# Kernel tuning notes

Measured on AMD Instinct MI355X. Metric: run time of the kernel, lower is better.

The kernel has to match this reference:

```python
import jax, jax.numpy as jnp
import numpy as np

N, F, H = 22, 448, 64
LN_EPS = 1e-5


def _layernorm(h, g, b):
    mu = h.mean(axis=-1, keepdims=True)
    var = ((h - mu) ** 2).mean(axis=-1, keepdims=True)
    return (h - mu) / jnp.sqrt(var + LN_EPS) * g + b


def setup_inputs() -> dict:
    key = jax.random.key(0)
    ks = jax.random.split(key, 16)
    B = 128
    x = jax.random.normal(ks[0], (B, N, F), dtype=jnp.float32)
    s = lambda fan_in: 1.0 / np.sqrt(fan_in)
    # correlation-branch edge_weight_net: Linear(2F,64) -> ReLU -> Linear(64,1) -> Sigmoid
    cw1 = jax.random.uniform(ks[1], (2 * F, 64), jnp.float32, -s(2 * F), s(2 * F))
    cb1 = jax.random.uniform(ks[2], (64,), jnp.float32, -s(2 * F), s(2 * F))
    cw2 = jax.random.uniform(ks[3], (64, 1), jnp.float32, -s(64), s(64))
    cb2 = jax.random.uniform(ks[4], (1,), jnp.float32, -s(64), s(64))
    # semantic branch
    emb = jax.random.normal(ks[5], (N, H), dtype=jnp.float32) * 0.01
    D = 2 * H + 2 * F
    sw1 = jax.random.uniform(ks[6], (D, H), jnp.float32, -s(D), s(D))
    sb1 = jax.random.uniform(ks[7], (H,), jnp.float32, -s(D), s(D))
    ln_g = jnp.ones((H,), jnp.float32)
    ln_b = jnp.zeros((H,), jnp.float32)
    sw2 = jax.random.uniform(ks[8], (H, H // 2), jnp.float32, -s(H), s(H))
    sb2 = jax.random.uniform(ks[9], (H // 2,), jnp.float32, -s(H), s(H))
    sw3 = jax.random.uniform(ks[10], (H // 2, 1), jnp.float32, -s(H // 2), s(H // 2))
    sb3 = jax.random.uniform(ks[11], (1,), jnp.float32, -s(H // 2), s(H // 2))
    thr = jnp.asarray(0.3, jnp.float32)
    alpha_p = jnp.asarray(0.6, jnp.float32)
    return dict(x=x, cw1=cw1, cb1=cb1, cw2=cw2, cb2=cb2, emb=emb,
                sw1=sw1, sb1=sb1, ln_g=ln_g, ln_b=ln_b,
                sw2=sw2, sb2=sb2, sw3=sw3, sb3=sb3,
                thr=thr, alpha_p=alpha_p)


def reference(x, cw1, cb1, cw2, cb2, emb, sw1, sb1, ln_g, ln_b,
              sw2, sb2, sw3, sb3, thr, alpha_p):
    B, n, f = x.shape
    eye = jnp.eye(n, dtype=x.dtype)[None]

    # ---- Correlation graph ----
    xc = x - x.mean(axis=-1, keepdims=True)
    std = jnp.std(x, axis=-1, ddof=1, keepdims=True) + 1e-8  # torch std is unbiased
    xn = xc / std
    corr = jnp.abs(jnp.einsum('bif,bjf->bij', xn, xn) / f)
    # pairwise edge features (B,N,N,2F)
    xi = jnp.broadcast_to(x[:, :, None, :], (B, n, n, f))
    xj = jnp.broadcast_to(x[:, None, :, :], (B, n, n, f))
    ef = jnp.concatenate([xi, xj], axis=-1)
    h = jax.nn.relu(ef @ cw1 + cb1)
    w_corr = jax.nn.sigmoid((h @ cw2 + cb2)[..., 0])
    g_corr = corr * w_corr + eye

    # ---- Semantic graph ----
    ei = jnp.broadcast_to(emb[None, :, None, :], (B, n, n, H))
    ej = jnp.broadcast_to(emb[None, None, :, :], (B, n, n, H))
    sf = jnp.concatenate([ei, ej, xi, xj], axis=-1)  # (B,N,N,2H+2F)
    h1 = jax.nn.relu(_layernorm(sf @ sw1 + sb1, ln_g, ln_b))
    h2 = jax.nn.relu(h1 @ sw2 + sb2)
    w_sem = jax.nn.sigmoid((h2 @ sw3 + sb3)[..., 0])  # (B,N,N)
    # original loop fills only i<j and mirrors; diagonal stays 0
    upper = jnp.triu(w_sem, k=1)
    adj = upper + jnp.swapaxes(upper, 1, 2)
    t = jax.nn.sigmoid(thr)
    adj = jnp.where(adj > t, adj, jnp.zeros_like(adj))
    g_sem = adj + eye

    # ---- Learned fusion ----
    alpha = jax.nn.sigmoid(alpha_p)
    return alpha * g_corr + (1.0 - alpha) * g_sem
```

## Files before the change

kernel.cpp:

```cpp
#include <hip/hip_runtime.h>
#include <math.h>

namespace {
constexpr int kN = 22;
constexpr int kF = 448;
constexpr int kNP = kN * kN;
constexpr int kXStr = 452;
constexpr int kSm1 = kN * kXStr + 2 * kN;
constexpr int kAStr = 36;
constexpr int kBStr = 68;
constexpr int kPStr = 68;
}

__global__ __launch_bounds__(256) void hgc_k1(
    const float* __restrict__ x,
    const float* __restrict__ cw1, const float* __restrict__ cb1,
    const float* __restrict__ emb,
    const float* __restrict__ sw1, const float* __restrict__ sb1,
    float* __restrict__ C, float* __restrict__ g,
    int M, int Mtiles, int nGemm)
{
    __shared__ __align__(16) float sm[kSm1];
    const int tid = threadIdx.x;

    if ((int)blockIdx.x < nGemm) {
        float* As = sm;
        float* Bs = sm + 64 * kAStr;
        const int bm = blockIdx.x % Mtiles;
        const int bn = blockIdx.x / Mtiles;
        const int m0 = bm * 32;

        const float* Wsrc =
            (bn == 0) ? cw1 :
            (bn == 1) ? cw1 + 448 * 64 :
            (bn == 2) ? sw1 + 128 * 64 :
                        sw1 + 576 * 64;

        const int tm = tid & 15;
        const int tn = tid >> 4;
        float acc[2][4];
        #pragma unroll
        for (int i = 0; i < 2; ++i)
            #pragma unroll
            for (int j = 0; j < 4; ++j) acc[i][j] = 0.f;

        for (int k0 = 0; k0 < kF; k0 += 64) {
            #pragma unroll
            for (int pass = 0; pass < 2; ++pass) {
                const int idx = tid + pass * 256;
                const int row = idx >> 4, kq = idx & 15;
                const int m = m0 + row;
                float4 v = {0, 0, 0, 0};
                if (m < M) v = *(const float4*)&x[(size_t)m * kF + k0 + kq * 4];
                As[(kq * 4 + 0) * kAStr + row] = v.x;
                As[(kq * 4 + 1) * kAStr + row] = v.y;
                As[(kq * 4 + 2) * kAStr + row] = v.z;
                As[(kq * 4 + 3) * kAStr + row] = v.w;
            }
            #pragma unroll
            for (int pass = 0; pass < 4; ++pass) {
                const int idx = tid + pass * 256;
                const int k = idx >> 4, nq = idx & 15;
                const float4 v = *(const float4*)&Wsrc[(size_t)(k0 + k) * 64 + nq * 4];
                *(float4*)&Bs[k * kBStr + nq * 4] = v;
            }
            __syncthreads();
            #pragma unroll 8
            for (int k = 0; k < 64; ++k) {
                const float2 a2 = *(const float2*)&As[k * kAStr + tm * 2];
                const float4 b4 = *(const float4*)&Bs[k * kBStr + tn * 4];
                acc[0][0] = fmaf(a2.x, b4.x, acc[0][0]);
                acc[0][1] = fmaf(a2.x, b4.y, acc[0][1]);
                acc[0][2] = fmaf(a2.x, b4.z, acc[0][2]);
                acc[0][3] = fmaf(a2.x, b4.w, acc[0][3]);
                acc[1][0] = fmaf(a2.y, b4.x, acc[1][0]);
                acc[1][1] = fmaf(a2.y, b4.y, acc[1][1]);
                acc[1][2] = fmaf(a2.y, b4.z, acc[1][2]);
                acc[1][3] = fmaf(a2.y, b4.w, acc[1][3]);
            }
            __syncthreads();
        }

        if (bn >= 2) {
            const float* W2 = sw1 + (bn == 2 ? 0 : 64) * 64;
            #pragma unroll
            for (int pass = 0; pass < 2; ++pass) {
                const int idx = tid + pass * 256;
                const int row = idx >> 4, kq = idx & 15;
                const int r = (m0 + row) % kN;
                const float4 v = *(const float4*)&emb[(size_t)r * 64 + kq * 4];
                As[(kq * 4 + 0) * kAStr + row] = v.x;
                As[(kq * 4 + 1) * kAStr + row] = v.y;
                As[(kq * 4 + 2) * kAStr + row] = v.z;
                As[(kq * 4 + 3) * kAStr + row] = v.w;
            }
            #pragma unroll
            for (int pass = 0; pass < 4; ++pass) {
                const int idx = tid + pass * 256;
                const int k = idx >> 4, nq = idx & 15;
                const float4 v = *(const float4*)&W2[(size_t)k * 64 + nq * 4];
                *(float4*)&Bs[k * kBStr + nq * 4] = v;
            }
            __syncthreads();
            #pragma unroll 8
            for (int k = 0; k < 64; ++k) {
                const float2 a2 = *(const float2*)&As[k * kAStr + tm * 2];
                const float4 b4 = *(const float4*)&Bs[k * kBStr + tn * 4];
                acc[0][0] = fmaf(a2.x, b4.x, acc[0][0]);
                acc[0][1] = fmaf(a2.x, b4.y, acc[0][1]);
                acc[0][2] = fmaf(a2.x, b4.z, acc[0][2]);
                acc[0][3] = fmaf(a2.x, b4.w, acc[0][3]);
                acc[1][0] = fmaf(a2.y, b4.x, acc[1][0]);
                acc[1][1] = fmaf(a2.y, b4.y, acc[1][1]);
                acc[1][2] = fmaf(a2.y, b4.z, acc[1][2]);
                acc[1][3] = fmaf(a2.y, b4.w, acc[1][3]);
            }
        }

        float4 bias = {0, 0, 0, 0};
        if (bn == 0)      bias = *(const float4*)&cb1[tn * 4];
        else if (bn == 2) bias = *(const float4*)&sb1[tn * 4];
        #pragma unroll
        for (int i = 0; i < 2; ++i) {
            const int m = m0 + tm * 2 + i;
            if (m < M) {
                float4 o;
                o.x = acc[i][0] + bias.x; o.y = acc[i][1] + bias.y;
                o.z = acc[i][2] + bias.z; o.w = acc[i][3] + bias.w;
                *(float4*)&C[(size_t)m * 256 + bn * 64 + tn * 4] = o;
            }
        }
    } else {
        float* smu = sm + kN * kXStr;
        float* sis = smu + kN;
        const int cb = blockIdx.x - nGemm;
        const int b = cb >> 1;
        const int r0 = (cb & 1) * 11;

        const float4* xb4 = (const float4*)(x + (size_t)b * (kN * kF));
        for (int idx = tid; idx < kN * kF / 4; idx += 256) {
            const float4 v = xb4[idx];
            const int r = idx / 112;
            const int k = (idx - r * 112) * 4;
            float* d = sm + r * kXStr + k;
            d[0] = v.x; d[1] = v.y; d[2] = v.z; d[3] = v.w;
        }
        __syncthreads();

        {
            const int wid = tid >> 6, lane = tid & 63;
            for (int r = wid; r < kN; r += 4) {
                const float* row = sm + r * kXStr;
                float s = 0.f;
                #pragma unroll
                for (int c = 0; c < 7; ++c) s += row[c * 64 + lane];
                #pragma unroll
                for (int o = 32; o; o >>= 1) s += __shfl_xor(s, o, 64);
                const float mean = s * (1.f / 448.f);
                float ss = 0.f;
                #pragma unroll
                for (int c = 0; c < 7; ++c) { const float d = row[c * 64 + lane] - mean; ss = fmaf(d, d, ss); }
                #pragma unroll
                for (int o = 32; o; o >>= 1) ss += __shfl_xor(ss, o, 64);
                if (lane == 0) {
                    smu[r] = mean;
                    sis[r] = 1.f / (sqrtf(ss * (1.f / 447.f)) + 1e-8f);
                }
            }
        }
        __syncthreads();

        for (int p = tid; p < 11 * kN; p += 256) {
            const int pi = p / 22;
            const int i = r0 + pi, j = p - pi * 22;
            const float4* ri = (const float4*)(sm + i * kXStr);
            const float4* rj = (const float4*)(sm + j * kXStr);
            float dot = 0.f;
            for (int q = 0; q < 112; ++q) {
                const float4 a = ri[q], bq = rj[q];
                dot = fmaf(a.x, bq.x, dot); dot = fmaf(a.y, bq.y, dot);
                dot = fmaf(a.z, bq.z, dot); dot = fmaf(a.w, bq.w, dot);
            }
            const float c = (dot - 448.f * smu[i] * smu[j]) * sis[i] * sis[j] * (1.f / 448.f);
            g[(size_t)b * kNP + i * 22 + j] = fabsf(c);
        }
    }
}

__global__ __launch_bounds__(256) void hgc_k2(
    const float* __restrict__ C, const float* __restrict__ g,
    const float* __restrict__ cw2, const float* __restrict__ cb2,
    const float* __restrict__ sw2, const float* __restrict__ sb2,
    const float* __restrict__ sw3, const float* __restrict__ sb3,
    const float* __restrict__ ln_g, const float* __restrict__ ln_b,
    const float* __restrict__ thr, const float* __restrict__ alpha_p,
    float* __restrict__ out)
{
    __shared__ __align__(16) float sp[4 * kN * kPStr];
    __shared__ float sg[kNP];
    __shared__ __align__(16) float sw2s[2048];
    __shared__ float scw2[64], slng[64], slnb[64], ssw3[32], ssb2[32];
    __shared__ float vbuf[32 * 66];

    const int tid = threadIdx.x;
    const int b   = blockIdx.x >> 2;
    const int pb  = blockIdx.x & 3;

    #pragma unroll
    for (int a = 0; a < 4; ++a) {
        float* dst = sp + a * kN * kPStr;
        for (int idx = tid; idx < 352; idx += 256) {
            const int r = idx >> 4, kq = idx & 15;
            const float4 v = *(const float4*)&C[((size_t)(b * 22 + r)) * 256 + a * 64 + kq * 4];
            *(float4*)&dst[r * kPStr + kq * 4] = v;
        }
    }
    for (int idx = tid; idx < kNP; idx += 256) sg[idx] = g[(size_t)b * kNP + idx];
    {
        const float4* s4 = (const float4*)sw2;
        for (int idx = tid; idx < 512; idx += 256)
            *((float4*)(sw2s + idx * 4)) = s4[idx];
    }
    if (tid < 64)       { scw2[tid] = cw2[tid]; slng[tid] = ln_g[tid]; slnb[tid] = ln_b[tid]; }
    else if (tid < 96)  { ssw3[tid - 64] = sw3[tid - 64]; }
    else if (tid < 128) { ssb2[tid - 96] = sb2[tid - 96]; }
    __syncthreads();

    const int pl = tid >> 3;
    const int t  = tid & 7;
    const float* sa1 = sp;
    const float* sa2 = sp + kN * kPStr;
    const float* su1 = sp + 2 * kN * kPStr;
    const float* su2 = sp + 3 * kN * kPStr;

    for (int ch = 0; ch < 4; ++ch) {
        const int lp = ch * 32 + pl;
        const bool valid = lp < 121;
        const int p = valid ? (pb * 121 + lp) : 0;
        const int i = p / 22, j = p - (p / 22) * 22;

        float zc = 0.f;
        {
            const float* pa1 = sa1 + i * kPStr + t * 8;
            const float* pa2 = sa2 + j * kPStr + t * 8;
            #pragma unroll
            for (int c = 0; c < 8; ++c) {
                const float h = fmaxf(pa1[c] + pa2[c], 0.f);
                zc = fmaf(h, scw2[t * 8 + c], zc);
            }
            zc += __shfl_xor(zc, 1, 64); zc += __shfl_xor(zc, 2, 64); zc += __shfl_xor(zc, 4, 64);
        }
        const float wc = 1.f / (1.f + __expf(-(zc + cb2[0])));

        const int lo = (i < j) ? i : j, hi = (i < j) ? j : i;
        const float* pu1 = su1 + lo * kPStr + t * 8;
        const float* pu2 = su2 + hi * kPStr + t * 8;
        float raw[8];
        float s1 = 0.f;
        #pragma unroll
        for (int c = 0; c < 8; ++c) { raw[c] = pu1[c] + pu2[c]; s1 += raw[c]; }
        s1 += __shfl_xor(s1, 1, 64); s1 += __shfl_xor(s1, 2, 64); s1 += __shfl_xor(s1, 4, 64);
        const float mean = s1 * (1.f / 64.f);
        float s2 = 0.f;
        #pragma unroll
        for (int c = 0; c < 8; ++c) { const float d = raw[c] - mean; s2 = fmaf(d, d, s2); }
        s2 += __shfl_xor(s2, 1, 64); s2 += __shfl_xor(s2, 2, 64); s2 += __shfl_xor(s2, 4, 64);
        const float rstd = rsqrtf(s2 * (1.f / 64.f) + 1e-5f);
        {
            float* vb = vbuf + pl * 66 + t * 8;
            #pragma unroll
            for (int c = 0; c < 8; ++c) {
                const int k = t * 8 + c;
                float v = (raw[c] - mean) * rstd;
                v = fmaf(v, slng[k], slnb[k]);
                vb[c] = fmaxf(v, 0.f);
            }
        }
        __syncthreads();

        float4 acc = {0, 0, 0, 0};
        {
            const float* vb = vbuf + pl * 66;
            for (int k = 0; k < 64; ++k) {
                const float v = vb[k];
                const float4 w = *((const float4*)(sw2s + k * 32 + t * 4));
                acc.x = fmaf(v, w.x, acc.x); acc.y = fmaf(v, w.y, acc.y);
                acc.z = fmaf(v, w.z, acc.z); acc.w = fmaf(v, w.w, acc.w);
            }
        }
        float z2;
        {
            const int o0 = t * 4;
            z2  = fmaxf(acc.x + ssb2[o0 + 0], 0.f) * ssw3[o0 + 0];
            z2 += fmaxf(acc.y + ssb2[o0 + 1], 0.f) * ssw3[o0 + 1];
            z2 += fmaxf(acc.z + ssb2[o0 + 2], 0.f) * ssw3[o0 + 2];
            z2 += fmaxf(acc.w + ssb2[o0 + 3], 0.f) * ssw3[o0 + 3];
            z2 += __shfl_xor(z2, 1, 64); z2 += __shfl_xor(z2, 2, 64); z2 += __shfl_xor(z2, 4, 64);
        }

        if (valid && t == 0) {
            float gsem;
            if (i == j) {
                gsem = 1.f;
            } else {
                const float wsem = 1.f / (1.f + expf(-(z2 + sb3[0])));
                const float tt   = 1.f / (1.f + expf(-thr[0]));
                gsem = (wsem > tt) ? wsem : 0.f;
            }
            const float alpha = 1.f / (1.f + __expf(-alpha_p[0]));
            const float gcorr = fmaf(sg[p], wc, (i == j) ? 1.f : 0.f);
            out[(size_t)b * kNP + p] = fmaf(alpha, gcorr, (1.f - alpha) * gsem);
        }
    }
}

extern "C" void kernel_launch(void* const* d_in, const int* in_sizes, int n_in,
                              void* d_out, int out_size, void* d_ws, size_t ws_size,
                              hipStream_t stream)
{
    (void)n_in; (void)out_size; (void)ws_size;
    const float* x     = (const float*)d_in[0];
    const float* cw1   = (const float*)d_in[1];
    const float* cb1   = (const float*)d_in[2];
    const float* cw2   = (const float*)d_in[3];
    const float* cb2   = (const float*)d_in[4];
    const float* emb   = (const float*)d_in[5];
    const float* sw1   = (const float*)d_in[6];
    const float* sb1   = (const float*)d_in[7];
    const float* ln_g  = (const float*)d_in[8];
    const float* ln_b  = (const float*)d_in[9];
    const float* sw2   = (const float*)d_in[10];
    const float* sb2   = (const float*)d_in[11];
    const float* sw3   = (const float*)d_in[12];
    const float* sb3   = (const float*)d_in[13];
    const float* thr   = (const float*)d_in[14];
    const float* alpha = (const float*)d_in[15];
    float* out = (float*)d_out;
    float* ws  = (float*)d_ws;

    const int B = in_sizes[0] / (kN * kF);
    const int M = kN * B;
    const int Mtiles = (M + 31) / 32;
    const int nGemm = Mtiles * 4;

    float* C = ws;
    float* g = ws + (size_t)M * 256;

    hipLaunchKernelGGL(hgc_k1, dim3(nGemm + 2 * B), dim3(256), 0, stream,
                       x, cw1, cb1, emb, sw1, sb1, C, g, M, Mtiles, nGemm);
    hipLaunchKernelGGL(hgc_k2, dim3(4 * B), dim3(256), 0, stream,
                       C, g, cw2, cb2, sw2, sb2, sw3, sb3, ln_g, ln_b, thr, alpha, out);
}
```

Before: 125.5 us.

## Enlarge GEMM tile with register prefetch and exploit pair symmetry in both kernels

After: 135.1 us. 1.08x slower.

```diff
diff --git a/kernel.cpp b/kernel.cpp
--- a/kernel.cpp
+++ b/kernel.cpp
@@ -7,9 +7,10 @@
 constexpr int kNP = kN * kN;
 constexpr int kXStr = 452;
 constexpr int kSm1 = kN * kXStr + 2 * kN;
-constexpr int kAStr = 36;
+constexpr int kAStr = 68;
 constexpr int kBStr = 68;
 constexpr int kPStr = 68;
+constexpr int kVStr = 68;
 }
 
 __global__ __launch_bounds__(256) void hgc_k1(
@@ -28,7 +29,7 @@
         float* Bs = sm + 64 * kAStr;
         const int bm = blockIdx.x % Mtiles;
         const int bn = blockIdx.x / Mtiles;
-        const int m0 = bm * 32;
+        const int m0 = bm * 64;
 
         const float* Wsrc =
             (bn == 0) ? cw1 :
@@ -38,82 +39,93 @@
 
         const int tm = tid & 15;
         const int tn = tid >> 4;
-        float acc[2][4];
+        const int ld_row = tid >> 4;
+        const int ld_kq  = tid & 15;
+
+        float acc[4][4];
         #pragma unroll
-        for (int i = 0; i < 2; ++i)
+        for (int i = 0; i < 4; ++i)
             #pragma unroll
             for (int j = 0; j < 4; ++j) acc[i][j] = 0.f;
 
+        float4 rA[4], rB[4];
+        #pragma unroll
+        for (int p = 0; p < 4; ++p) {
+            const int row = ld_row + p * 16;
+            int m = m0 + row; if (m >= M) m = M - 1;
+            rA[p] = *(const float4*)&x[(size_t)m * kF + ld_kq * 4];
+            rB[p] = *(const float4*)&Wsrc[(size_t)row * 64 + ld_kq * 4];
+        }
+
         for (int k0 = 0; k0 < kF; k0 += 64) {
             #pragma unroll
-            for (int pass = 0; pass < 2; ++pass) {
-                const int idx = tid + pass * 256;
-                const int row = idx >> 4, kq = idx & 15;
-                const int m = m0 + row;
-                float4 v = {0, 0, 0, 0};
-                if (m < M) v = *(const float4*)&x[(size_t)m * kF + k0 + kq * 4];
-                As[(kq * 4 + 0) * kAStr + row] = v.x;
-                As[(kq * 4 + 1) * kAStr + row] = v.y;
-                As[(kq * 4 + 2) * kAStr + row] = v.z;
-                As[(kq * 4 + 3) * kAStr + row] = v.w;
-            }
+            for (int p = 0; p < 4; ++p) {
+                const int row = ld_row + p * 16;
+                As[(ld_kq * 4 + 0) * kAStr + row] = rA[p].x;
+                As[(ld_kq * 4 + 1) * kAStr + row] = rA[p].y;
+                As[(ld_kq * 4 + 2) * kAStr + row] = rA[p].z;
+                As[(ld_kq * 4 + 3) * kAStr + row] = rA[p].w;
+                *(float4*)&Bs[row * kBStr + ld_kq * 4] = rB[p];
+            }
+            __syncthreads();
+            const int kn = k0 + 64;
+            if (kn < kF) {
+                #pragma unroll
+                for (int p = 0; p < 4; ++p) {
+                    const int row = ld_row + p * 16;
+                    int m = m0 + row; if (m >= M) m = M - 1;
+                    rA[p] = *(const float4*)&x[(size_t)m * kF + kn + ld_kq * 4];
+                    rB[p] = *(const float4*)&Wsrc[(size_t)(kn + row) * 64 + ld_kq * 4];
+                }
+            } else if (bn >= 2) {
+                const float* W2 = sw1 + (bn == 2 ? 0 : 64) * 64;
+                #pragma unroll
+                for (int p = 0; p < 4; ++p) {
+                    const int row = ld_row + p * 16;
+                    const int r = (m0 + row) % kN;
+                    rA[p] = *(const float4*)&emb[(size_t)r * 64 + ld_kq * 4];
+                    rB[p] = *(const float4*)&W2[(size_t)row * 64 + ld_kq * 4];
+                }
+            }
+            #pragma unroll 8
+            for (int k = 0; k < 64; ++k) {
+                const float4 a4 = *(const float4*)&As[k * kAStr + tm * 4];
+                const float4 b4 = *(const float4*)&Bs[k * kBStr + tn * 4];
+                acc[0][0] = fmaf(a4.x, b4.x, acc[0][0]); acc[0][1] = fmaf(a4.x, b4.y, acc[0][1]);
+                acc[0][2] = fmaf(a4.x, b4.z, acc[0][2]); acc[0][3] = fmaf(a4.x, b4.w, acc[0][3]);
+                acc[1][0] = fmaf(a4.y, b4.x, acc[1][0]); acc[1][1] = fmaf(a4.y, b4.y, acc[1][1]);
+                acc[1][2] = fmaf(a4.y, b4.z, acc[1][2]); acc[1][3] = fmaf(a4.y, b4.w, acc[1][3]);
+                acc[2][0] = fmaf(a4.z, b4.x, acc[2][0]); acc[2][1] = fmaf(a4.z, b4.y, acc[2][1]);
+                acc[2][2] = fmaf(a4.z, b4.z, acc[2][2]); acc[2][3] = fmaf(a4.z, b4.w, acc[2][3]);
+                acc[3][0] = fmaf(a4.w, b4.x, acc[3][0]); acc[3][1] = fmaf(a4.w, b4.y, acc[3][1]);
+                acc[3][2] = fmaf(a4.w, b4.z, acc[3][2]); acc[3][3] = fmaf(a4.w, b4.w, acc[3][3]);
+            }
+            __syncthreads();
+        }
+
+        if (bn >= 2) {
             #pragma unroll
-            for (int pass = 0; pass < 4; ++pass) {
-                const int idx = tid + pass * 256;
-                const int k = idx >> 4, nq = idx & 15;
-                const float4 v = *(const float4*)&Wsrc[(size_t)(k0 + k) * 64 + nq * 4];
-                *(float4*)&Bs[k * kBStr + nq * 4] = v;
+            for (int p = 0; p < 4; ++p) {
+                const int row = ld_row + p * 16;
+                As[(ld_kq * 4 + 0) * kAStr + row] = rA[p].x;
+                As[(ld_kq * 4 + 1) * kAStr + row] = rA[p].y;
+                As[(ld_kq * 4 + 2) * kAStr + row] = rA[p].z;
+                As[(ld_kq * 4 + 3) * kAStr + row] = rA[p].w;
+                *(float4*)&Bs[row * kBStr + ld_kq * 4] = rB[p];
             }
             __syncthreads();
             #pragma unroll 8
             for (int k = 0; k < 64; ++k) {
-                const float2 a2 = *(const float2*)&As[k * kAStr + tm * 2];
+                const float4 a4 = *(const float4*)&As[k * kAStr + tm * 4];
                 const float4 b4 = *(const float4*)&Bs[k * kBStr + tn * 4];
-                acc[0][0] = fmaf(a2.x, b4.x, acc[0][0]);
-                acc[0][1] = fmaf(a2.x, b4.y, acc[0][1]);
-                acc[0][2] = fmaf(a2.x, b4.z, acc[0][2]);
-                acc[0][3] = fmaf(a2.x, b4.w, acc[0][3]);
-                acc[1][0] = fmaf(a2.y, b4.x, acc[1][0]);
-                acc[1][1] = fmaf(a2.y, b4.y, acc[1][1]);
-                acc[1][2] = fmaf(a2.y, b4.z, acc[1][2]);
-                acc[1][3] = fmaf(a2.y, b4.w, acc[1][3]);
-            }
-            __syncthreads();
-        }
-
-        if (bn >= 2) {
-            const float* W2 = sw1 + (bn == 2 ? 0 : 64) * 64;
-            #pragma unroll
-            for (int pass = 0; pass < 2; ++pass) {
-                const int idx = tid + pass * 256;
-                const int row = idx >> 4, kq = idx & 15;
-                const int r = (m0 + row) % kN;
-                const float4 v = *(const float4*)&emb[(size_t)r * 64 + kq * 4];
-                As[(kq * 4 + 0) * kAStr + row] = v.x;
-                As[(kq * 4 + 1) * kAStr + row] = v.y;
-                As[(kq * 4 + 2) * kAStr + row] = v.z;
-                As[(kq * 4 + 3) * kAStr + row] = v.w;
-            }
-            #pragma unroll
-            for (int pass = 0; pass < 4; ++pass) {
-                const int idx = tid + pass * 256;
-                const int k = idx >> 4, nq = idx & 15;
-                const float4 v = *(const float4*)&W2[(size_t)k * 64 + nq * 4];
-                *(float4*)&Bs[k * kBStr + nq * 4] = v;
-            }
-            __syncthreads();
-            #pragma unroll 8
-            for (int k = 0; k < 64; ++k) {
-                const float2 a2 = *(const float2*)&As[k * kAStr + tm * 2];
-                const float4 b4 = *(const float4*)&Bs[k * kBStr + tn * 4];
-                acc[0][0] = fmaf(a2.x, b4.x, acc[0][0]);
-                acc[0][1] = fmaf(a2.x, b4.y, acc[0][1]);
-                acc[0][2] = fmaf(a2.x, b4.z, acc[0][2]);
-                acc[0][3] = fmaf(a2.x, b4.w, acc[0][3]);
-                acc[1][0] = fmaf(a2.y, b4.x, acc[1][0]);
-                acc[1][1] = fmaf(a2.y, b4.y, acc[1][1]);
-                acc[1][2] = fmaf(a2.y, b4.z, acc[1][2]);
-                acc[1][3] = fmaf(a2.y, b4.w, acc[1][3]);
+                acc[0][0] = fmaf(a4.x, b4.x, acc[0][0]); acc[0][1] = fmaf(a4.x, b4.y, acc[0][1]);
+                acc[0][2] = fmaf(a4.x, b4.z, acc[0][2]); acc[0][3] = fmaf(a4.x, b4.w, acc[0][3]);
+                acc[1][0] = fmaf(a4.y, b4.x, acc[1][0]); acc[1][1] = fmaf(a4.y, b4.y, acc[1][1]);
+                acc[1][2] = fmaf(a4.y, b4.z, acc[1][2]); acc[1][3] = fmaf(a4.y, b4.w, acc[1][3]);
+                acc[2][0] = fmaf(a4.z, b4.x, acc[2][0]); acc[2][1] = fmaf(a4.z, b4.y, acc[2][1]);
+                acc[2][2] = fmaf(a4.z, b4.z, acc[2][2]); acc[2][3] = fmaf(a4.z, b4.w, acc[2][3]);
+                acc[3][0] = fmaf(a4.w, b4.x, acc[3][0]); acc[3][1] = fmaf(a4.w, b4.y, acc[3][1]);
+                acc[3][2] = fmaf(a4.w, b4.z, acc[3][2]); acc[3][3] = fmaf(a4.w, b4.w, acc[3][3]);
             }
         }
 
@@ -121,8 +133,8 @@
         if (bn == 0)      bias = *(const float4*)&cb1[tn * 4];
         else if (bn == 2) bias = *(const float4*)&sb1[tn * 4];
         #pragma unroll
-        for (int i = 0; i < 2; ++i) {
-            const int m = m0 + tm * 2 + i;
+        for (int i = 0; i < 4; ++i) {
+            const int m = m0 + tm * 4 + i;
             if (m < M) {
                 float4 o;
                 o.x = acc[i][0] + bias.x; o.y = acc[i][1] + bias.y;
@@ -133,9 +145,7 @@
     } else {
         float* smu = sm + kN * kXStr;
         float* sis = smu + kN;
-        const int cb = blockIdx.x - nGemm;
-        const int b = cb >> 1;
-        const int r0 = (cb & 1) * 11;
+        const int b = blockIdx.x - nGemm;
 
         const float4* xb4 = (const float4*)(x + (size_t)b * (kN * kF));
         for (int idx = tid; idx < kN * kF / 4; idx += 256) {
@@ -170,9 +180,10 @@
         }
         __syncthreads();
 
-        for (int p = tid; p < 11 * kN; p += 256) {
-            const int pi = p / 22;
-            const int i = r0 + pi, j = p - pi * 22;
+        if (tid < 253) {
+            int rem = tid, i = 0;
+            while (rem >= kN - i) { rem -= kN - i; ++i; }
+            const int j = i + rem;
             const float4* ri = (const float4*)(sm + i * kXStr);
             const float4* rj = (const float4*)(sm + j * kXStr);
             float dot = 0.f;
@@ -182,7 +193,9 @@
                 dot = fmaf(a.z, bq.z, dot); dot = fmaf(a.w, bq.w, dot);
             }
             const float c = (dot - 448.f * smu[i] * smu[j]) * sis[i] * sis[j] * (1.f / 448.f);
-            g[(size_t)b * kNP + i * 22 + j] = fabsf(c);
+            const float ac = fabsf(c);
+            g[(size_t)b * kNP + i * 22 + j] = ac;
+            g[(size_t)b * kNP + j * 22 + i] = ac;
         }
     }
 }
@@ -200,11 +213,11 @@
     __shared__ float sg[kNP];
     __shared__ __align__(16) float sw2s[2048];
     __shared__ float scw2[64], slng[64], slnb[64], ssw3[32], ssb2[32];
-    __shared__ float vbuf[32 * 66];
+    __shared__ __align__(16) float vbuf[32 * kVStr];
 
     const int tid = threadIdx.x;
-    const int b   = blockIdx.x >> 2;
-    const int pb  = blockIdx.x & 3;
+    const int b   = blockIdx.x >> 1;
+    const int pb  = blockIdx.x & 1;
 
     #pragma unroll
     for (int a = 0; a < 4; ++a) {
@@ -234,31 +247,60 @@
     const float* su2 = sp + 3 * kN * kPStr;
 
     for (int ch = 0; ch < 4; ++ch) {
-        const int lp = ch * 32 + pl;
-        const bool valid = lp < 121;
-        const int p = valid ? (pb * 121 + lp) : 0;
-        const int i = p / 22, j = p - (p / 22) * 22;
-
-        float zc = 0.f;
-        {
-            const float* pa1 = sa1 + i * kPStr + t * 8;
-            const float* pa2 = sa2 + j * kPStr + t * 8;
-            #pragma unroll
-            for (int c = 0; c < 8; ++c) {
-                const float h = fmaxf(pa1[c] + pa2[c], 0.f);
-                zc = fmaf(h, scw2[t * 8 + c], zc);
-            }
-            zc += __shfl_xor(zc, 1, 64); zc += __shfl_xor(zc, 2, 64); zc += __shfl_xor(zc, 4, 64);
-        }
-        const float wc = 1.f / (1.f + __expf(-(zc + cb2[0])));
-
-        const int lo = (i < j) ? i : j, hi = (i < j) ? j : i;
-        const float* pu1 = su1 + lo * kPStr + t * 8;
-        const float* pu2 = su2 + hi * kPStr + t * 8;
+        const int s_  = pb * 128 + ch * 32 + pl;
+        const bool valid = s_ < 253;
+        const int s = valid ? s_ : 252;
+        int i, j;
+        if (s < 231) {
+            int rem = s, i0 = 0;
+            while (rem >= 21 - i0) { rem -= 21 - i0; ++i0; }
+            i = i0; j = i0 + 1 + rem;
+        } else { i = j = s - 231; }
+
+        float zc1 = 0.f, zc2 = 0.f;
+        {
+            const float* a1i = sa1 + i * kPStr + t * 8;
+            const float* a2j = sa2 + j * kPStr + t * 8;
+            const float* a1j = sa1 + j * kPStr + t * 8;
+            const float* a2i = sa2 + i * kPStr + t * 8;
+            const float4 i0 = *(const float4*)a1i, i1 = *(const float4*)(a1i + 4);
+            const float4 j0 = *(const float4*)a2j, j1 = *(const float4*)(a2j + 4);
+            const float4 k0 = *(const float4*)a1j, k1 = *(const float4*)(a1j + 4);
+            const float4 l0 = *(const float4*)a2i, l1 = *(const float4*)(a2i + 4);
+            const float4 w0 = *(const float4*)(scw2 + t * 8);
+            const float4 w1 = *(const float4*)(scw2 + t * 8 + 4);
+            zc1 = fmaf(fmaxf(i0.x + j0.x, 0.f), w0.x, zc1);
+            zc1 = fmaf(fmaxf(i0.y + j0.y, 0.f), w0.y, zc1);
+            zc1 = fmaf(fmaxf(i0.z + j0.z, 0.f), w0.z, zc1);
+            zc1 = fmaf(fmaxf(i0.w + j0.w, 0.f), w0.w, zc1);
+            zc1 = fmaf(fmaxf(i1.x + j1.x, 0.f), w1.x, zc1);
+            zc1 = fmaf(fmaxf(i1.y + j1.y, 0.f), w1.y, zc1);
+            zc1 = fmaf(fmaxf(i1.z + j1.z, 0.f), w1.z, zc1);
+            zc1 = fmaf(fmaxf(i1.w + j1.w, 0.f), w1.w, zc1);
+            zc2 = fmaf(fmaxf(k0.x + l0.x, 0.f), w0.x, zc2);
+            zc2 = fmaf(fmaxf(k0.y + l0.y, 0.f), w0.y, zc2);
+            zc2 = fmaf(fmaxf(k0.z + l0.z, 0.f), w0.z, zc2);
+            zc2 = fmaf(fmaxf(k0.w + l0.w, 0.f), w0.w, zc2);
+            zc2 = fmaf(fmaxf(k1.x + l1.x, 0.f), w1.x, zc2);
+            zc2 = fmaf(fmaxf(k1.y + l1.y, 0.f), w1.y, zc2);
+            zc2 = fmaf(fmaxf(k1.z + l1.z, 0.f), w1.z, zc2);
+            zc2 = fmaf(fmaxf(k1.w + l1.w, 0.f), w1.w, zc2);
+            zc1 += __shfl_xor(zc1, 1, 64); zc1 += __shfl_xor(zc1, 2, 64); zc1 += __shfl_xor(zc1, 4, 64);
+            zc2 += __shfl_xor(zc2, 1, 64); zc2 += __shfl_xor(zc2, 2, 64); zc2 += __shfl_xor(zc2, 4, 64);
+        }
+
         float raw[8];
         float s1 = 0.f;
-        #pragma unroll
-        for (int c = 0; c < 8; ++c) { raw[c] = pu1[c] + pu2[c]; s1 += raw[c]; }
+        {
+            const float* pu1 = su1 + i * kPStr + t * 8;
+            const float* pu2 = su2 + j * kPStr + t * 8;
+            const float4 u0 = *(const float4*)pu1, u1v = *(const float4*)(pu1 + 4);
+            const float4 v0 = *(const float4*)pu2, v1v = *(const float4*)(pu2 + 4);
+            raw[0] = u0.x + v0.x; raw[1] = u0.y + v0.y; raw[2] = u0.z + v0.z; raw[3] = u0.w + v0.w;
+            raw[4] = u1v.x + v1v.x; raw[5] = u1v.y + v1v.y; raw[6] = u1v.z + v1v.z; raw[7] = u1v.w + v1v.w;
+            #pragma unroll
+            for (int c = 0; c < 8; ++c) s1 += raw[c];
+        }
         s1 += __shfl_xor(s1, 1, 64); s1 += __shfl_xor(s1, 2, 64); s1 += __shfl_xor(s1, 4, 64);
         const float mean = s1 * (1.f / 64.f);
         float s2 = 0.f;
@@ -267,20 +309,24 @@
         s2 += __shfl_xor(s2, 1, 64); s2 += __shfl_xor(s2, 2, 64); s2 += __shfl_xor(s2, 4, 64);
         const float rstd = rsqrtf(s2 * (1.f / 64.f) + 1e-5f);
         {
-            float* vb = vbuf + pl * 66 + t * 8;
-            #pragma unroll
-            for (int c = 0; c < 8; ++c) {
-                const int k = t * 8 + c;
-                float v = (raw[c] - mean) * rstd;
-                v = fmaf(v, slng[k], slnb[k]);
-                vb[c] = fmaxf(v, 0.f);
-            }
+            float* vb = vbuf + pl * kVStr + t * 8;
+            float4 o0, o1;
+            o0.x = fmaxf(fmaf((raw[0] - mean) * rstd, slng[t*8+0], slnb[t*8+0]), 0.f);
+            o0.y = fmaxf(fmaf((raw[1] - mean) * rstd, slng[t*8+1], slnb[t*8+1]), 0.f);
+            o0.z = fmaxf(fmaf((raw[2] - mean) * rstd, slng[t*8+2], slnb[t*8+2]), 0.f);
+            o0.w = fmaxf(fmaf((raw[3] - mean) * rstd, slng[t*8+3], slnb[t*8+3]), 0.f);
+            o1.x = fmaxf(fmaf((raw[4] - mean) * rstd, slng[t*8+4], slnb[t*8+4]), 0.f);
+            o1.y = fmaxf(fmaf((raw[5] - mean) * rstd, slng[t*8+5], slnb[t*8+5]), 0.f);
+            o1.z = fmaxf(fmaf((raw[6] - mean) * rstd, slng[t*8+6], slnb[t*8+6]), 0.f);
+            o1.w = fmaxf(fmaf((raw[7] - mean) * rstd, slng[t*8+7], slnb[t*8+7]), 0.f);
+            *(float4*)vb = o0;
+            *(float4*)(vb + 4) = o1;
         }
         __syncthreads();
 
         float4 acc = {0, 0, 0, 0};
         {
-            const float* vb = vbuf + pl * 66;
+            const float* vb = vbuf + pl * kVStr;
             for (int k = 0; k < 64; ++k) {
                 const float v = vb[k];
                 const float4 w = *((const float4*)(sw2s + k * 32 + t * 4));
@@ -299,6 +345,8 @@
         }
 
         if (valid && t == 0) {
+            const float alpha = 1.f / (1.f + __expf(-alpha_p[0]));
+            const float wc_ij = 1.f / (1.f + __expf(-(zc1 + cb2[0])));
             float gsem;
             if (i == j) {
                 gsem = 1.f;
@@ -307,10 +355,15 @@
                 const float tt   = 1.f / (1.f + expf(-thr[0]));
                 gsem = (wsem > tt) ? wsem : 0.f;
             }
-            const float alpha = 1.f / (1.f + __expf(-alpha_p[0]));
-            const float gcorr = fmaf(sg[p], wc, (i == j) ? 1.f : 0.f);
-            out[(size_t)b * kNP + p] = fmaf(alpha, gcorr, (1.f - alpha) * gsem);
-        }
+            const float gc_ij = fmaf(sg[i * 22 + j], wc_ij, (i == j) ? 1.f : 0.f);
+            out[(size_t)b * kNP + i * 22 + j] = fmaf(alpha, gc_ij, (1.f - alpha) * gsem);
+            if (i != j) {
+                const float wc_ji = 1.f / (1.f + __expf(-(zc2 + cb2[0])));
+                const float gc_ji = sg[j * 22 + i] * wc_ji;
+                out[(size_t)b * kNP + j * 22 + i] = fmaf(alpha, gc_ji, (1.f - alpha) * gsem);
+            }
+        }
+        __syncthreads();
     }
 }
 
@@ -340,14 +393,14 @@
 
     const int B = in_sizes[0] / (kN * kF);
     const int M = kN * B;
-    const int Mtiles = (M + 31) / 32;
+    const int Mtiles = (M + 63) / 64;
     const int nGemm = Mtiles * 4;
 
     float* C = ws;
     float* g = ws + (size_t)M * 256;
 
-    hipLaunchKernelGGL(hgc_k1, dim3(nGemm + 2 * B), dim3(256), 0, stream,
+    hipLaunchKernelGGL(hgc_k1, dim3(nGemm + B), dim3(256), 0, stream,
                        x, cw1, cb1, emb, sw1, sb1, C, g, M, Mtiles, nGemm);
-    hipLaunchKernelGGL(hgc_k2, dim3(4 * B), dim3(256), 0, stream,
+    hipLaunchKernelGGL(hgc_k2, dim3(2 * B), dim3(256), 0, stream,
                        C, g, cw2, cb2, sw2, sb2, sw3, sb3, ln_g, ln_b, thr, alpha, out);
 }
```
